# Kernel optimization log

Hardware: AMD Instinct MI355X
Metric: run time of the kernel (lower is better)

Reference implementation:

```python
import jax, jax.numpy as jnp
import numpy as np

NUM_HEADS = 12
HEAD_DIM = 64
DIM = 768


def _rot_interleaved(t):
    # rot(x): pairs (x0,x1) -> (-x1, x0), interleaved layout
    x1 = t[..., ::2]
    x2 = t[..., 1::2]
    return jnp.stack([-x2, x1], axis=-1).reshape(t.shape)


def _apply_rope_cat(t, emb):
    # emb: [N, 2*head_dim] = concat(sin, cos); t: [B, H, N, head_dim]
    sin_e, cos_e = jnp.split(emb, 2, axis=-1)  # each [N, head_dim]
    return t * cos_e + _rot_interleaved(t) * sin_e


def setup_inputs() -> dict:
    key = jax.random.key(0)
    ks = jax.random.split(key, 8)
    B, Nq, Nkv = 16, 256, 4096
    s = 1.0 / np.sqrt(DIM)
    return {
        "x": jax.random.normal(ks[0], (B, Nq, DIM), dtype=jnp.float32),
        "context": jax.random.normal(ks[1], (B, Nkv, DIM), dtype=jnp.float32),
        "rope_q": jax.random.normal(ks[2], (Nq, 2 * HEAD_DIM), dtype=jnp.float32),
        "rope_k": jax.random.normal(ks[3], (Nkv, 2 * HEAD_DIM), dtype=jnp.float32),
        "Wq": jax.random.normal(ks[4], (DIM, DIM), dtype=jnp.float32) * s,
        "Wk": jax.random.normal(ks[5], (DIM, DIM), dtype=jnp.float32) * s,
        "Wv": jax.random.normal(ks[6], (DIM, DIM), dtype=jnp.float32) * s,
        "Wo": jax.random.normal(ks[7], (DIM, DIM), dtype=jnp.float32) * s,
    }


def reference(x, context, rope_q, rope_k, Wq, Wk, Wv, Wo):
    B, Nq, _ = x.shape
    Nkv = context.shape[1]
    H, hd = NUM_HEADS, HEAD_DIM
    scale = hd ** -0.5

    # projections -> [B, H, N, hd]
    q = jnp.einsum('bnd,df->bnf', x, Wq).reshape(B, Nq, H, hd).transpose(0, 2, 1, 3)
    k = jnp.einsum('bnd,df->bnf', context, Wk).reshape(B, Nkv, H, hd).transpose(0, 2, 1, 3)
    v = jnp.einsum('bnd,df->bnf', context, Wv).reshape(B, Nkv, H, hd).transpose(0, 2, 1, 3)

    q = _apply_rope_cat(q, rope_q)
    k = _apply_rope_cat(k, rope_k)

    attn = jnp.einsum('bhqd,bhkd->bhqk', q * scale, k)
    attn = jax.nn.softmax(attn, axis=-1)
    o = jnp.einsum('bhqk,bhkd->bhqd', attn, v)  # [B, H, Nq, hd]
    o = o.transpose(0, 2, 1, 3).reshape(B, Nq, H * hd)
    return jnp.einsum('bnf,fo->bno', o, Wo)
```

## Files before the change

### kernel.cpp

```cpp
#include <hip/hip_runtime.h>
#include <stdint.h>


typedef __bf16 bf16x8 __attribute__((ext_vector_type(8)));
typedef unsigned short u16x8 __attribute__((ext_vector_type(8)));
typedef unsigned short u16x4 __attribute__((ext_vector_type(4)));
typedef uint32_t u32x4 __attribute__((ext_vector_type(4)));
typedef float f32x4 __attribute__((ext_vector_type(4)));

#define DIMF 768
#define NHEAD 12
#define NKV 4096
#define NQ 256
#define NB 16

struct alignas(8) us4 { unsigned short x, y, z, w; };

__device__ __forceinline__ unsigned short f2bf(float x) {
  uint32_t u = __float_as_uint(x);
  u += 0x7fffu + ((u >> 16) & 1u);
  return (unsigned short)(u >> 16);
}

__global__ void cvt_kernel(const float* __restrict__ in, unsigned short* __restrict__ out, int n) {
  int stride = gridDim.x * blockDim.x * 4;
  for (int i = (blockIdx.x * blockDim.x + threadIdx.x) * 4; i < n; i += stride) {
    float4 v = *(const float4*)(in + i);
    us4 o{f2bf(v.x), f2bf(v.y), f2bf(v.z), f2bf(v.w)};
    *(us4*)(out + i) = o;
  }
}

__global__ void twt_kernel(const float* __restrict__ W0, const float* __restrict__ W1,
                           const float* __restrict__ W2, const float* __restrict__ W3,
                           unsigned short* __restrict__ O0, unsigned short* __restrict__ O1,
                           unsigned short* __restrict__ O2, unsigned short* __restrict__ O3) {
  const float* W; unsigned short* O;
  switch (blockIdx.z) {
    case 0: W = W0; O = O0; break;
    case 1: W = W1; O = O1; break;
    case 2: W = W2; O = O2; break;
    default: W = W3; O = O3; break;
  }
  __shared__ float t[32][33];
  int x0 = blockIdx.x * 32, y0 = blockIdx.y * 32;
  int tx = threadIdx.x, ty = threadIdx.y;
#pragma unroll
  for (int j = 0; j < 4; ++j)
    t[ty + 8 * j][tx] = W[(size_t)(y0 + ty + 8 * j) * DIMF + x0 + tx];
  __syncthreads();
#pragma unroll
  for (int j = 0; j < 4; ++j)
    O[(size_t)(x0 + ty + 8 * j) * DIMF + y0 + tx] = f2bf(t[tx][ty + 8 * j]);
}

template <int MODE>
__launch_bounds__(256, 2)
__global__ void gemm_kernel(const unsigned short* __restrict__ A,
                            const unsigned short* __restrict__ Bt,
                            void* __restrict__ outp,
                            const float* __restrict__ rope) {
  __shared__ unsigned short As[128 * 64];
  __shared__ unsigned short Bs[128 * 64];
  const int t = threadIdx.x;
  const int lane = t & 63, wid = t >> 6;
  const int g = lane >> 4, lc = lane & 15;
  const int wr = wid >> 1, wc = wid & 1;
  const int rowBase = blockIdx.x * 128, colBase = blockIdx.y * 128;

  const f32x4 z4 = {0.f, 0.f, 0.f, 0.f};
  f32x4 acc[4][4];
#pragma unroll
  for (int m = 0; m < 4; ++m)
#pragma unroll
    for (int n = 0; n < 4; ++n) acc[m][n] = z4;

  const int r0 = t >> 3;
  const int c0 = t & 7;

  bf16x8 ra[4], rb[4];
#pragma unroll
  for (int pp = 0; pp < 4; ++pp) {
    int row = pp * 32 + r0;
    ra[pp] = *(const bf16x8*)(A + (size_t)(rowBase + row) * DIMF + c0 * 8);
    rb[pp] = *(const bf16x8*)(Bt + (size_t)(colBase + row) * DIMF + c0 * 8);
  }

  for (int kb = 0; kb < 12; ++kb) {
    __syncthreads();
#pragma unroll
    for (int pp = 0; pp < 4; ++pp) {
      int row = pp * 32 + r0;
      int ph = ((c0 ^ (row & 7)) << 3);
      *(bf16x8*)&As[row * 64 + ph] = ra[pp];
      *(bf16x8*)&Bs[row * 64 + ph] = rb[pp];
    }
    __syncthreads();
    if (kb + 1 < 12) {
      int kn = (kb + 1) * 64;
#pragma unroll
      for (int pp = 0; pp < 4; ++pp) {
        int row = pp * 32 + r0;
        ra[pp] = *(const bf16x8*)(A + (size_t)(rowBase + row) * DIMF + kn + c0 * 8);
        rb[pp] = *(const bf16x8*)(Bt + (size_t)(colBase + row) * DIMF + kn + c0 * 8);
      }
    }
#pragma unroll
    for (int kk = 0; kk < 2; ++kk) {
      bf16x8 af[4], bfr[4];
#pragma unroll
      for (int m = 0; m < 4; ++m) {
        int row = wr * 64 + m * 16 + lc;
        int ch = kk * 4 + g;
        af[m] = *(const bf16x8*)&As[row * 64 + (((ch ^ (row & 7))) << 3)];
      }
#pragma unroll
      for (int n = 0; n < 4; ++n) {
        int row = wc * 64 + n * 16 + lc;
        int ch = kk * 4 + g;
        bfr[n] = *(const bf16x8*)&Bs[row * 64 + (((ch ^ (row & 7))) << 3)];
      }
#pragma unroll
      for (int m = 0; m < 4; ++m)
#pragma unroll
        for (int n = 0; n < 4; ++n)
          acc[m][n] = __builtin_amdgcn_mfma_f32_16x16x32_bf16(af[m], bfr[n], acc[m][n], 0, 0, 0);
    }
  }

  if (MODE == 0 || MODE == 2) {
    unsigned short* Ko = (unsigned short*)outp;
#pragma unroll
    for (int m = 0; m < 4; ++m)
#pragma unroll
      for (int n = 0; n < 4; ++n)
#pragma unroll
        for (int r = 0; r < 4; ++r) {
          int p = rowBase + wr * 64 + m * 16 + g * 4 + r;
          int f = colBase + wc * 64 + n * 16 + lc;
          int d = f & 63, h = f >> 6;
          float v = acc[m][n][r];
          float vo = __shfl_xor(v, 1);
          if (MODE == 0) {
            int b = p >> 12, nkv = p & 4095;
            float sn = rope[nkv * 128 + d], cs = rope[nkv * 128 + 64 + d];
            float o = (d & 1) ? fmaf(vo, sn, v * cs) : fmaf(-vo, sn, v * cs);
            Ko[((size_t)(b * NHEAD + h) * NKV + nkv) * 64 + d] = f2bf(o);
          } else {
            int b = p >> 8, nq = p & 255;
            float sn = rope[nq * 128 + d], cs = rope[nq * 128 + 64 + d];
            float o = (d & 1) ? fmaf(vo, sn, v * cs) : fmaf(-vo, sn, v * cs);
            Ko[((size_t)(b * NHEAD + h) * NQ + nq) * 64 + d] = f2bf(o * 0.125f);
          }
        }
  } else if (MODE == 1) {
    unsigned short* Vt = (unsigned short*)outp;
#pragma unroll
    for (int m = 0; m < 4; ++m)
#pragma unroll
      for (int n = 0; n < 4; ++n) {
        int p0 = rowBase + wr * 64 + m * 16 + g * 4;
        int b = p0 >> 12, nkv0 = p0 & 4095;
        int f = colBase + wc * 64 + n * 16 + lc;
        int d = f & 63, h = f >> 6;
        us4 wv{f2bf(acc[m][n][0]), f2bf(acc[m][n][1]), f2bf(acc[m][n][2]), f2bf(acc[m][n][3])};
        *(us4*)&Vt[((size_t)(b * NHEAD + h) * 64 + d) * NKV + nkv0] = wv;
      }
  } else {
    float* Co = (float*)outp;
#pragma unroll
    for (int m = 0; m < 4; ++m)
#pragma unroll
      for (int n = 0; n < 4; ++n)
#pragma unroll
        for (int r = 0; r < 4; ++r) {
          int p = rowBase + wr * 64 + m * 16 + g * 4 + r;
          int f = colBase + wc * 64 + n * 16 + lc;
          Co[(size_t)p * DIMF + f] = acc[m][n][r];
        }
  }
}

__launch_bounds__(256, 2)
__global__ void attn_kernel(const unsigned short* __restrict__ Qb,
                            const unsigned short* __restrict__ Kb,
                            const unsigned short* __restrict__ Vtb,
                            unsigned short* __restrict__ Ob) {
  __shared__ unsigned short Ks[128 * 64];
  __shared__ unsigned short Vts[64 * 128];
  const int logical = (blockIdx.x & 7) * 96 + (blockIdx.x >> 3);
  const int qt = logical & 3, bh = logical >> 2;
  const int b = bh / NHEAD, h = bh % NHEAD;
  const int t = threadIdx.x;
  const int lane = t & 63, w = t >> 6;
  const int g = lane >> 4, lc = lane & 15;
  const int qrow = qt * 64 + w * 16 + lc;

  bf16x8 qf[2];
#pragma unroll
  for (int kk = 0; kk < 2; ++kk)
    qf[kk] = *(const bf16x8*)(Qb + ((size_t)bh * NQ + qrow) * 64 + kk * 32 + g * 8);

  const f32x4 z4 = {0.f, 0.f, 0.f, 0.f};
  f32x4 oacc[4];
#pragma unroll
  for (int df = 0; df < 4; ++df) oacc[df] = z4;
  float mrun = -1e30f, lrun = 0.f;

  const int r0 = t >> 3, c0 = t & 7;
  const int d0 = t >> 4, cv = t & 15;
  const int pbase = 32 * (cv >> 2) + 16 * (cv & 1) + 4 * ((cv >> 1) & 1);
  const int ch0 = pbase >> 3, of0 = pbase & 7;
  const int ch1 = (pbase + 8) >> 3;

  u16x8 rk[4], rv[4];
#define LOAD_TILE(KT)                                                                        \
  do {                                                                                       \
    const int kvb = (KT) * 128;                                                              \
    _Pragma("unroll")                                                                        \
    for (int pp = 0; pp < 4; ++pp)                                                           \
      rk[pp] = *(const u16x8*)(Kb + ((size_t)bh * NKV + kvb + pp * 32 + r0) * 64 + c0 * 8);  \
    _Pragma("unroll")                                                                        \
    for (int pp = 0; pp < 4; ++pp)                                                           \
      rv[pp] = *(const u16x8*)(Vtb + ((size_t)bh * 64 + pp * 16 + d0) * NKV + kvb + cv * 8); \
  } while (0)

  LOAD_TILE(0);

  for (int kt = 0; kt < 32; ++kt) {
    __syncthreads();
#pragma unroll
    for (int pp = 0; pp < 4; ++pp) {
      int row = pp * 32 + r0;
      *(u16x8*)&Ks[row * 64 + ((c0 ^ (row & 7)) << 3)] = rk[pp];
    }
#pragma unroll
    for (int pp = 0; pp < 4; ++pp) {
      int d = pp * 16 + d0;
      u16x4 lo = __builtin_shufflevector(rv[pp], rv[pp], 0, 1, 2, 3);
      u16x4 hi = __builtin_shufflevector(rv[pp], rv[pp], 4, 5, 6, 7);
      *(u16x4*)&Vts[d * 128 + ((ch0 ^ (d & 15)) << 3) + of0] = lo;
      *(u16x4*)&Vts[d * 128 + ((ch1 ^ (d & 15)) << 3) + of0] = hi;
    }
    if (kt + 1 < 32) LOAD_TILE(kt + 1);
    __syncthreads();

    f32x4 s[8];
#pragma unroll
    for (int c = 0; c < 8; ++c) s[c] = z4;
#pragma unroll
    for (int kk = 0; kk < 2; ++kk)
#pragma unroll
      for (int c = 0; c < 8; ++c) {
        int row = c * 16 + lc;
        bf16x8 kf = *(const bf16x8*)&Ks[row * 64 + (((kk * 4 + g) ^ (row & 7)) << 3)];
        s[c] = __builtin_amdgcn_mfma_f32_16x16x32_bf16(kf, qf[kk], s[c], 0, 0, 0);
      }

    float mx = s[0][0];
#pragma unroll
    for (int c = 0; c < 8; ++c)
#pragma unroll
      for (int r = 0; r < 4; ++r) mx = fmaxf(mx, s[c][r]);
    mx = fmaxf(mx, __shfl_xor(mx, 16));
    mx = fmaxf(mx, __shfl_xor(mx, 32));
    float nm = fmaxf(mrun, mx);
    float al = __expf(mrun - nm);
    mrun = nm;
    float ls = 0.f;
#pragma unroll
    for (int c = 0; c < 8; ++c)
#pragma unroll
      for (int r = 0; r < 4; ++r) {
        float p = __expf(s[c][r] - nm);
        s[c][r] = p;
        ls += p;
      }
    ls += __shfl_xor(ls, 16);
    ls += __shfl_xor(ls, 32);
    lrun = lrun * al + ls;
#pragma unroll
    for (int df = 0; df < 4; ++df)
#pragma unroll
      for (int r = 0; r < 4; ++r) oacc[df][r] *= al;

    uint32_t pk[8][2];
#pragma unroll
    for (int c = 0; c < 8; ++c)
#pragma unroll
      for (int w2 = 0; w2 < 2; ++w2) {
        float a = s[c][2 * w2], bb = s[c][2 * w2 + 1];
        asm("v_cvt_pk_bf16_f32 %0, %1, %2" : "=v"(pk[c][w2]) : "v"(a), "v"(bb));
      }

#pragma unroll
    for (int kb = 0; kb < 4; ++kb) {
      u32x4 pw = {pk[2 * kb][0], pk[2 * kb][1], pk[2 * kb + 1][0], pk[2 * kb + 1][1]};
      bf16x8 pa = __builtin_bit_cast(bf16x8, pw);
#pragma unroll
      for (int df = 0; df < 4; ++df) {
        int row = df * 16 + lc;
        bf16x8 vf = *(const bf16x8*)&Vts[row * 128 + (((kb * 4 + g) ^ (row & 15)) << 3)];
        oacc[df] = __builtin_amdgcn_mfma_f32_16x16x32_bf16(vf, pa, oacc[df], 0, 0, 0);
      }
    }
  }
#undef LOAD_TILE

  float inv = 1.0f / lrun;
#pragma unroll
  for (int df = 0; df < 4; ++df) {
    us4 wv{f2bf(oacc[df][0] * inv), f2bf(oacc[df][1] * inv),
           f2bf(oacc[df][2] * inv), f2bf(oacc[df][3] * inv)};
    *(us4*)&Ob[((size_t)b * NQ + qrow) * DIMF + h * 64 + df * 16 + g * 4] = wv;
  }
}

extern "C" void kernel_launch(void* const* d_in, const int* in_sizes, int n_in,
                              void* d_out, int out_size, void* d_ws, size_t ws_size,
                              hipStream_t stream) {
  const float* x      = (const float*)d_in[0];
  const float* ctx    = (const float*)d_in[1];
  const float* rope_q = (const float*)d_in[2];
  const float* rope_k = (const float*)d_in[3];
  const float* Wq     = (const float*)d_in[4];
  const float* Wk     = (const float*)d_in[5];
  const float* Wv     = (const float*)d_in[6];
  const float* Wo     = (const float*)d_in[7];

  char* ws = (char*)d_ws;
  const size_t SZ_CTXB = (size_t)NB * NKV * DIMF * 2;
  const size_t SZ_XB   = (size_t)NB * NQ * DIMF * 2;
  const size_t SZ_WT   = (size_t)DIMF * DIMF * 2;
  unsigned short* ctxb = (unsigned short*)(ws);
  unsigned short* ob   = (unsigned short*)(ws);
  unsigned short* xb   = (unsigned short*)(ws + SZ_CTXB);
  unsigned short* wkt  = (unsigned short*)(ws + SZ_CTXB + SZ_XB);
  unsigned short* wvt  = (unsigned short*)(ws + SZ_CTXB + SZ_XB + SZ_WT);
  unsigned short* wqt  = (unsigned short*)(ws + SZ_CTXB + SZ_XB + 2 * SZ_WT);
  unsigned short* wot  = (unsigned short*)(ws + SZ_CTXB + SZ_XB + 3 * SZ_WT);
  unsigned short* kb   = (unsigned short*)(ws + SZ_CTXB + SZ_XB + 4 * SZ_WT);
  unsigned short* vtb  = (unsigned short*)(ws + SZ_CTXB + SZ_XB + 4 * SZ_WT + SZ_CTXB);
  unsigned short* qb   = (unsigned short*)(ws + SZ_CTXB + SZ_XB + 4 * SZ_WT + 2 * SZ_CTXB);

  cvt_kernel<<<dim3(2048), dim3(256), 0, stream>>>(ctx, ctxb, NB * NKV * DIMF);
  cvt_kernel<<<dim3(1024), dim3(256), 0, stream>>>(x, xb, NB * NQ * DIMF);
  twt_kernel<<<dim3(24, 24, 4), dim3(32, 8), 0, stream>>>(Wk, Wv, Wq, Wo, wkt, wvt, wqt, wot);

  gemm_kernel<0><<<dim3(512, 6), dim3(256), 0, stream>>>(ctxb, wkt, kb, rope_k);
  gemm_kernel<1><<<dim3(512, 6), dim3(256), 0, stream>>>(ctxb, wvt, vtb, nullptr);
  gemm_kernel<2><<<dim3(32, 6), dim3(256), 0, stream>>>(xb, wqt, qb, rope_q);

  attn_kernel<<<dim3(768), dim3(256), 0, stream>>>(qb, kb, vtb, ob);

  gemm_kernel<3><<<dim3(32, 6), dim3(256), 0, stream>>>(ob, wot, d_out, nullptr);
}
```

Baseline: 408.9 us.

## Load GEMM tiles directly into LDS with global_load_lds, dropping register staging

Replaces the register-staged, XOR-swizzled global-to-LDS tile copy in the projection GEMM with direct global_load_lds transfers of 16 bytes per lane. This removes the register round-trip and the VGPRs used for staging. It also drops both the register-level prefetch of the next K block and the LDS swizzle. The unswizzled layout risks LDS bank conflicts on fragment reads, and loads are no longer overlapped with MFMA compute across iterations.

```diff
diff --git a/kernel.cpp b/kernel.cpp
--- a/kernel.cpp
+++ b/kernel.cpp
@@ -20,6 +20,12 @@
   uint32_t u = __float_as_uint(x);
   u += 0x7fffu + ((u >> 16) & 1u);
   return (unsigned short)(u >> 16);
+}
+
+__device__ __forceinline__ void gld_lds16(const unsigned short* g, unsigned short* l) {
+  __builtin_amdgcn_global_load_lds(
+      (const __attribute__((address_space(1))) uint32_t*)(uintptr_t)g,
+      (__attribute__((address_space(3))) uint32_t*)(uintptr_t)l, 16, 0, 0);
 }
 
 __global__ void cvt_kernel(const float* __restrict__ in, unsigned short* __restrict__ out, int n) {
@@ -75,51 +81,28 @@
 #pragma unroll
     for (int n = 0; n < 4; ++n) acc[m][n] = z4;
 
-  const int r0 = t >> 3;
-  const int c0 = t & 7;
-
-  bf16x8 ra[4], rb[4];
-#pragma unroll
-  for (int pp = 0; pp < 4; ++pp) {
-    int row = pp * 32 + r0;
-    ra[pp] = *(const bf16x8*)(A + (size_t)(rowBase + row) * DIMF + c0 * 8);
-    rb[pp] = *(const bf16x8*)(Bt + (size_t)(colBase + row) * DIMF + c0 * 8);
-  }
+  const int srow = wid * 32 + (lane >> 3);
+  const int schk = lane & 7;
 
   for (int kb = 0; kb < 12; ++kb) {
     __syncthreads();
-#pragma unroll
-    for (int pp = 0; pp < 4; ++pp) {
-      int row = pp * 32 + r0;
-      int ph = ((c0 ^ (row & 7)) << 3);
-      *(bf16x8*)&As[row * 64 + ph] = ra[pp];
-      *(bf16x8*)&Bs[row * 64 + ph] = rb[pp];
+    const unsigned short* Ab = A + (size_t)(rowBase + srow) * DIMF + kb * 64 + schk * 8;
+    const unsigned short* Bb = Bt + (size_t)(colBase + srow) * DIMF + kb * 64 + schk * 8;
+#pragma unroll
+    for (int i = 0; i < 4; ++i) {
+      gld_lds16(Ab + (size_t)i * 8 * DIMF, &As[(wid * 32 + i * 8) * 64]);
+      gld_lds16(Bb + (size_t)i * 8 * DIMF, &Bs[(wid * 32 + i * 8) * 64]);
     }
     __syncthreads();
-    if (kb + 1 < 12) {
-      int kn = (kb + 1) * 64;
-#pragma unroll
-      for (int pp = 0; pp < 4; ++pp) {
-        int row = pp * 32 + r0;
-        ra[pp] = *(const bf16x8*)(A + (size_t)(rowBase + row) * DIMF + kn + c0 * 8);
-        rb[pp] = *(const bf16x8*)(Bt + (size_t)(colBase + row) * DIMF + kn + c0 * 8);
-      }
-    }
 #pragma unroll
     for (int kk = 0; kk < 2; ++kk) {
       bf16x8 af[4], bfr[4];
 #pragma unroll
-      for (int m = 0; m < 4; ++m) {
-        int row = wr * 64 + m * 16 + lc;
-        int ch = kk * 4 + g;
-        af[m] = *(const bf16x8*)&As[row * 64 + (((ch ^ (row & 7))) << 3)];
-      }
-#pragma unroll
-      for (int n = 0; n < 4; ++n) {
-        int row = wc * 64 + n * 16 + lc;
-        int ch = kk * 4 + g;
-        bfr[n] = *(const bf16x8*)&Bs[row * 64 + (((ch ^ (row & 7))) << 3)];
-      }
+      for (int m = 0; m < 4; ++m)
+        af[m] = *(const bf16x8*)&As[(wr * 64 + m * 16 + lc) * 64 + (kk * 4 + g) * 8];
+#pragma unroll
+      for (int n = 0; n < 4; ++n)
+        bfr[n] = *(const bf16x8*)&Bs[(wc * 64 + n * 16 + lc) * 64 + (kk * 4 + g) * 8];
 #pragma unroll
       for (int m = 0; m < 4; ++m)
 #pragma unroll
```

Result: slower. 422.5 us (+3.3%).

## Fuse K and V projections with fp32-to-bf16 context conversion in one kernel

Applied to the files above, without the earlier changes.

Replaces the separate context conversion pass and the two K and V GEMM launches with one kernel. It reads fp32 context directly, converts it to bf16 while staging into shared memory, and computes the K and V column tiles together in 512-thread blocks so each context tile is loaded once. Block indices are swizzled to improve cache locality of the weights. This removes the bf16 context round trip through global memory and the duplicated context reads, at the cost of more shared memory and register pressure per block and fp32 loads (twice the bytes) inside the GEMM loop.

```diff
diff --git a/kernel.cpp b/kernel.cpp
--- a/kernel.cpp
+++ b/kernel.cpp
@@ -20,6 +20,12 @@
   uint32_t u = __float_as_uint(x);
   u += 0x7fffu + ((u >> 16) & 1u);
   return (unsigned short)(u >> 16);
+}
+
+__device__ __forceinline__ uint32_t cvtpk(float a, float b) {
+  uint32_t r;
+  asm("v_cvt_pk_bf16_f32 %0, %1, %2" : "=v"(r) : "v"(a), "v"(b));
+  return r;
 }
 
 __global__ void cvt_kernel(const float* __restrict__ in, unsigned short* __restrict__ out, int n) {
@@ -52,6 +58,126 @@
 #pragma unroll
   for (int j = 0; j < 4; ++j)
     O[(size_t)(x0 + ty + 8 * j) * DIMF + y0 + tx] = f2bf(t[tx][ty + 8 * j]);
+}
+
+__launch_bounds__(512, 4)
+__global__ void kvproj_kernel(const float* __restrict__ ctx,
+                              const unsigned short* __restrict__ wkt,
+                              const unsigned short* __restrict__ wvt,
+                              unsigned short* __restrict__ Ko,
+                              unsigned short* __restrict__ Vt,
+                              const float* __restrict__ rope) {
+  __shared__ unsigned short As[128 * 64];
+  __shared__ unsigned short Bs[256 * 64];
+  const int t = threadIdx.x;
+  const int lane = t & 63, wid = t >> 6;
+  const int g = lane >> 4, lc = lane & 15;
+  const int wr = wid >> 2, wc = wid & 3;
+
+  const int bid = blockIdx.x;
+  const int swz = (bid & 7) * 384 + (bid >> 3);
+  const int cg = swz % 6;
+  const int rowBase = (swz / 6) * 128;
+  const int colBase = cg * 128;
+
+  const f32x4 z4 = {0.f, 0.f, 0.f, 0.f};
+  f32x4 acc[4][4];
+#pragma unroll
+  for (int m = 0; m < 4; ++m)
+#pragma unroll
+    for (int n = 0; n < 4; ++n) acc[m][n] = z4;
+
+  const int ar = t >> 2, ac = t & 3;
+  const int br = t >> 1, bc = t & 1;
+  const unsigned short* Bsrc = (br < 128)
+      ? wkt + (size_t)(colBase + br) * DIMF
+      : wvt + (size_t)(colBase + br - 128) * DIMF;
+
+  f32x4 fa[4];
+  u16x8 rb[4];
+
+#define LOAD_STEP(KB)                                                          \
+  do {                                                                         \
+    const float* Ab = ctx + (size_t)(rowBase + ar) * DIMF + (KB) * 64 + ac * 16; \
+    _Pragma("unroll")                                                          \
+    for (int i = 0; i < 4; ++i) fa[i] = *(const f32x4*)(Ab + 4 * i);           \
+    const unsigned short* Bb = Bsrc + (KB) * 64 + bc * 32;                     \
+    _Pragma("unroll")                                                          \
+    for (int i = 0; i < 4; ++i) rb[i] = *(const u16x8*)(Bb + 8 * i);           \
+  } while (0)
+
+  LOAD_STEP(0);
+
+  for (int kb = 0; kb < 12; ++kb) {
+    __syncthreads();
+#pragma unroll
+    for (int j = 0; j < 2; ++j) {
+      u32x4 pw = {cvtpk(fa[2 * j][0], fa[2 * j][1]),
+                  cvtpk(fa[2 * j][2], fa[2 * j][3]),
+                  cvtpk(fa[2 * j + 1][0], fa[2 * j + 1][1]),
+                  cvtpk(fa[2 * j + 1][2], fa[2 * j + 1][3])};
+      int c = ac * 2 + j;
+      *(u32x4*)&As[ar * 64 + ((c ^ (ar & 7)) << 3)] = pw;
+    }
+#pragma unroll
+    for (int i = 0; i < 4; ++i) {
+      int c = bc * 4 + i;
+      *(u16x8*)&Bs[br * 64 + ((c ^ (br & 7)) << 3)] = rb[i];
+    }
+    __syncthreads();
+    if (kb + 1 < 12) LOAD_STEP(kb + 1);
+#pragma unroll
+    for (int kk = 0; kk < 2; ++kk) {
+      bf16x8 af[4], bfr[4];
+#pragma unroll
+      for (int m = 0; m < 4; ++m) {
+        int row = wr * 64 + m * 16 + lc;
+        af[m] = *(const bf16x8*)&As[row * 64 + (((kk * 4 + g) ^ (row & 7)) << 3)];
+      }
+#pragma unroll
+      for (int n = 0; n < 4; ++n) {
+        int row = wc * 64 + n * 16 + lc;
+        bfr[n] = *(const bf16x8*)&Bs[row * 64 + (((kk * 4 + g) ^ (row & 7)) << 3)];
+      }
+#pragma unroll
+      for (int m = 0; m < 4; ++m)
+#pragma unroll
+        for (int n = 0; n < 4; ++n)
+          acc[m][n] = __builtin_amdgcn_mfma_f32_16x16x32_bf16(af[m], bfr[n], acc[m][n], 0, 0, 0);
+    }
+  }
+#undef LOAD_STEP
+
+  if (wc < 2) {
+#pragma unroll
+    for (int m = 0; m < 4; ++m)
+#pragma unroll
+      for (int n = 0; n < 4; ++n)
+#pragma unroll
+        for (int r = 0; r < 4; ++r) {
+          int p = rowBase + wr * 64 + m * 16 + g * 4 + r;
+          int f = colBase + wc * 64 + n * 16 + lc;
+          int d = f & 63, h = f >> 6;
+          float v = acc[m][n][r];
+          float vo = __shfl_xor(v, 1);
+          int b = p >> 12, nkv = p & 4095;
+          float sn = rope[nkv * 128 + d], cs = rope[nkv * 128 + 64 + d];
+          float o = (d & 1) ? fmaf(vo, sn, v * cs) : fmaf(-vo, sn, v * cs);
+          Ko[((size_t)(b * NHEAD + h) * NKV + nkv) * 64 + d] = f2bf(o);
+        }
+  } else {
+#pragma unroll
+    for (int m = 0; m < 4; ++m)
+#pragma unroll
+      for (int n = 0; n < 4; ++n) {
+        int p0 = rowBase + wr * 64 + m * 16 + g * 4;
+        int b = p0 >> 12, nkv0 = p0 & 4095;
+        int f = colBase + (wc - 2) * 64 + n * 16 + lc;
+        int d = f & 63, h = f >> 6;
+        us4 wv{f2bf(acc[m][n][0]), f2bf(acc[m][n][1]), f2bf(acc[m][n][2]), f2bf(acc[m][n][3])};
+        *(us4*)&Vt[((size_t)(b * NHEAD + h) * 64 + d) * NKV + nkv0] = wv;
+      }
+  }
 }
 
 template <int MODE>
@@ -78,12 +204,12 @@
   const int r0 = t >> 3;
   const int c0 = t & 7;
 
-  bf16x8 ra[4], rb[4];
+  bf16x8 ra[4], rbx[4];
 #pragma unroll
   for (int pp = 0; pp < 4; ++pp) {
     int row = pp * 32 + r0;
     ra[pp] = *(const bf16x8*)(A + (size_t)(rowBase + row) * DIMF + c0 * 8);
-    rb[pp] = *(const bf16x8*)(Bt + (size_t)(colBase + row) * DIMF + c0 * 8);
+    rbx[pp] = *(const bf16x8*)(Bt + (size_t)(colBase + row) * DIMF + c0 * 8);
   }
 
   for (int kb = 0; kb < 12; ++kb) {
@@ -93,7 +219,7 @@
       int row = pp * 32 + r0;
       int ph = ((c0 ^ (row & 7)) << 3);
       *(bf16x8*)&As[row * 64 + ph] = ra[pp];
-      *(bf16x8*)&Bs[row * 64 + ph] = rb[pp];
+      *(bf16x8*)&Bs[row * 64 + ph] = rbx[pp];
     }
     __syncthreads();
     if (kb + 1 < 12) {
@@ -102,7 +228,7 @@
       for (int pp = 0; pp < 4; ++pp) {
         int row = pp * 32 + r0;
         ra[pp] = *(const bf16x8*)(A + (size_t)(rowBase + row) * DIMF + kn + c0 * 8);
-        rb[pp] = *(const bf16x8*)(Bt + (size_t)(colBase + row) * DIMF + kn + c0 * 8);
+        rbx[pp] = *(const bf16x8*)(Bt + (size_t)(colBase + row) * DIMF + kn + c0 * 8);
       }
     }
 #pragma unroll
@@ -128,7 +254,7 @@
     }
   }
 
-  if (MODE == 0 || MODE == 2) {
+  if (MODE == 2) {
     unsigned short* Ko = (unsigned short*)outp;
 #pragma unroll
     for (int m = 0; m < 4; ++m)
@@ -141,31 +267,11 @@
           int d = f & 63, h = f >> 6;
           float v = acc[m][n][r];
           float vo = __shfl_xor(v, 1);
-          if (MODE == 0) {
-            int b = p >> 12, nkv = p & 4095;
-            float sn = rope[nkv * 128 + d], cs = rope[nkv * 128 + 64 + d];
-            float o = (d & 1) ? fmaf(vo, sn, v * cs) : fmaf(-vo, sn, v * cs);
-            Ko[((size_t)(b * NHEAD + h) * NKV + nkv) * 64 + d] = f2bf(o);
-          } else {
-            int b = p >> 8, nq = p & 255;
-            float sn = rope[nq * 128 + d], cs = rope[nq * 128 + 64 + d];
-            float o = (d & 1) ? fmaf(vo, sn, v * cs) : fmaf(-vo, sn, v * cs);
-            Ko[((size_t)(b * NHEAD + h) * NQ + nq) * 64 + d] = f2bf(o * 0.125f);
-          }
+          int b = p >> 8, nq = p & 255;
+          float sn = rope[nq * 128 + d], cs = rope[nq * 128 + 64 + d];
+          float o = (d & 1) ? fmaf(vo, sn, v * cs) : fmaf(-vo, sn, v * cs);
+          Ko[((size_t)(b * NHEAD + h) * NQ + nq) * 64 + d] = f2bf(o * 0.125f);
         }
-  } else if (MODE == 1) {
-    unsigned short* Vt = (unsigned short*)outp;
-#pragma unroll
-    for (int m = 0; m < 4; ++m)
-#pragma unroll
-      for (int n = 0; n < 4; ++n) {
-        int p0 = rowBase + wr * 64 + m * 16 + g * 4;
-        int b = p0 >> 12, nkv0 = p0 & 4095;
-        int f = colBase + wc * 64 + n * 16 + lc;
-        int d = f & 63, h = f >> 6;
-        us4 wv{f2bf(acc[m][n][0]), f2bf(acc[m][n][1]), f2bf(acc[m][n][2]), f2bf(acc[m][n][3])};
-        *(us4*)&Vt[((size_t)(b * NHEAD + h) * 64 + d) * NKV + nkv0] = wv;
-      }
   } else {
     float* Co = (float*)outp;
 #pragma unroll
@@ -288,10 +394,8 @@
 #pragma unroll
     for (int c = 0; c < 8; ++c)
 #pragma unroll
-      for (int w2 = 0; w2 < 2; ++w2) {
-        float a = s[c][2 * w2], bb = s[c][2 * w2 + 1];
-        asm("v_cvt_pk_bf16_f32 %0, %1, %2" : "=v"(pk[c][w2]) : "v"(a), "v"(bb));
-      }
+      for (int w2 = 0; w2 < 2; ++w2)
+        pk[c][w2] = cvtpk(s[c][2 * w2], s[c][2 * w2 + 1]);
 
 #pragma unroll
     for (int kb = 0; kb < 4; ++kb) {
@@ -332,7 +436,6 @@
   const size_t SZ_CTXB = (size_t)NB * NKV * DIMF * 2;
   const size_t SZ_XB   = (size_t)NB * NQ * DIMF * 2;
   const size_t SZ_WT   = (size_t)DIMF * DIMF * 2;
-  unsigned short* ctxb = (unsigned short*)(ws);
   unsigned short* ob   = (unsigned short*)(ws);
   unsigned short* xb   = (unsigned short*)(ws + SZ_CTXB);
   unsigned short* wkt  = (unsigned short*)(ws + SZ_CTXB + SZ_XB);
@@ -343,12 +446,10 @@
   unsigned short* vtb  = (unsigned short*)(ws + SZ_CTXB + SZ_XB + 4 * SZ_WT + SZ_CTXB);
   unsigned short* qb   = (unsigned short*)(ws + SZ_CTXB + SZ_XB + 4 * SZ_WT + 2 * SZ_CTXB);
 
-  cvt_kernel<<<dim3(2048), dim3(256), 0, stream>>>(ctx, ctxb, NB * NKV * DIMF);
   cvt_kernel<<<dim3(1024), dim3(256), 0, stream>>>(x, xb, NB * NQ * DIMF);
   twt_kernel<<<dim3(24, 24, 4), dim3(32, 8), 0, stream>>>(Wk, Wv, Wq, Wo, wkt, wvt, wqt, wot);
 
-  gemm_kernel<0><<<dim3(512, 6), dim3(256), 0, stream>>>(ctxb, wkt, kb, rope_k);
-  gemm_kernel<1><<<dim3(512, 6), dim3(256), 0, stream>>>(ctxb, wvt, vtb, nullptr);
+  kvproj_kernel<<<dim3(3072), dim3(512), 0, stream>>>(ctx, wkt, wvt, kb, vtb, rope_k);
   gemm_kernel<2><<<dim3(32, 6), dim3(256), 0, stream>>>(xb, wqt, qb, rope_q);
 
   attn_kernel<<<dim3(768), dim3(256), 0, stream>>>(qb, kb, vtb, ob);
```

Result: slower. 431.1 us (+5.4%).
